# Kernel optimization log

Measured on AMD Instinct MI355X. Metric: run time of the kernel, lower is better.

## Reference

```python
import jax, jax.numpy as jnp
import numpy as np

N = 100000
E = 1600000
F_IN = 128
HID = 16
HEADS = 8
NCLS = 2
NGRAPH = 64
NEG_SLOPE = 0.2


def setup_inputs() -> dict:
    key = jax.random.key(0)
    ks = jax.random.split(key, 12)
    x = jax.random.normal(ks[0], (N, F_IN), dtype=jnp.float32)
    edge_index = jax.random.randint(ks[1], (2, E), 0, N, dtype=jnp.int64)
    batch = jnp.sort(jax.random.randint(ks[2], (N,), 0, NGRAPH, dtype=jnp.int64))
    s1 = 1.0 / np.sqrt(F_IN)
    s2 = 1.0 / np.sqrt(HEADS * HID)
    W1 = jax.random.normal(ks[3], (F_IN, HEADS * HID), dtype=jnp.float32) * s1
    att_src1 = jax.random.normal(ks[4], (HEADS, HID), dtype=jnp.float32) * s2
    att_dst1 = jax.random.normal(ks[5], (HEADS, HID), dtype=jnp.float32) * s2
    b1 = jnp.zeros((HEADS * HID,), dtype=jnp.float32)
    W2 = jax.random.normal(ks[6], (HEADS * HID, 1 * NCLS), dtype=jnp.float32) * s2
    att_src2 = jax.random.normal(ks[7], (1, NCLS), dtype=jnp.float32)
    att_dst2 = jax.random.normal(ks[8], (1, NCLS), dtype=jnp.float32)
    b2 = jnp.zeros((NCLS,), dtype=jnp.float32)
    return {"x": x, "edge_index": edge_index, "batch": batch,
            "W1": W1, "att_src1": att_src1, "att_dst1": att_dst1, "b1": b1,
            "W2": W2, "att_src2": att_src2, "att_dst2": att_dst2, "b2": b2}


def _gat_conv(x, src, dst, W, att_src, att_dst, bias, heads, out_dim, concat):
    # x: [N, Fin]; src/dst: [E'] (self-loops already appended)
    h = (x @ W).reshape(N, heads, out_dim)              # [N, H, D]
    a_src = jnp.sum(h * att_src[None], axis=-1)          # [N, H]
    a_dst = jnp.sum(h * att_dst[None], axis=-1)          # [N, H]
    e = a_src[src] + a_dst[dst]                          # [E', H]
    e = jnp.where(e >= 0, e, NEG_SLOPE * e)              # leaky_relu
    # softmax over incoming edges of each destination node
    emax = jax.ops.segment_max(e, dst, num_segments=N)   # [N, H]
    ee = jnp.exp(e - emax[dst])
    denom = jax.ops.segment_sum(ee, dst, num_segments=N)
    alpha = ee / denom[dst]                              # [E', H]
    msg = h[src] * alpha[:, :, None]                     # [E', H, D]
    out = jax.ops.segment_sum(msg, dst, num_segments=N)  # [N, H, D]
    if concat:
        out = out.reshape(N, heads * out_dim)
    else:
        out = out.mean(axis=1)
    return out + bias


def reference(x, edge_index, batch, W1, att_src1, att_dst1, b1, W2, att_src2, att_dst2, b2):
    # add self-loops (PyG GATConv default add_self_loops=True)
    loop = jnp.arange(N, dtype=edge_index.dtype)
    src = jnp.concatenate([edge_index[0], loop])
    dst = jnp.concatenate([edge_index[1], loop])

    h = _gat_conv(x, src, dst, W1, att_src1, att_dst1, b1, HEADS, HID, True)
    h = jax.nn.elu(h)
    h = _gat_conv(h, src, dst, W2, att_src2, att_dst2, b2, 1, NCLS, False)

    # global mean pool over graphs
    ssum = jax.ops.segment_sum(h, batch, num_segments=NGRAPH)          # [G, C]
    cnt = jax.ops.segment_sum(jnp.ones((N,), h.dtype), batch, num_segments=NGRAPH)
    pooled = ssum / jnp.maximum(cnt, 1.0)[:, None]
    return jax.nn.log_softmax(pooled, axis=1)
```

## Files before the change

kernel.cpp:

```cpp
#include <hip/hip_runtime.h>
#include <math.h>

typedef long long ll;
typedef unsigned int u32;
typedef unsigned short u16;

#define NBLK 256
#define MAXBUK 512

__device__ __forceinline__ int load_idx(const void* p, int i, int is64) {
  return is64 ? (int)((const ll*)p)[i] : ((const int*)p)[i];
}

__device__ __forceinline__ u16 f2bf(float f) {
  u32 u = __float_as_uint(f);
  u += 0x7FFFu + ((u >> 16) & 1u);
  return (u16)(u >> 16);
}

__global__ void detect_kernel(const void* __restrict__ eidx, int ne,
                              const void* __restrict__ batch, int nb,
                              int* __restrict__ flags) {
  if (threadIdx.x == 0 && blockIdx.x == 0) {
    int e64 = 1;
    for (int k = 1; k <= 16; ++k) {
      int i = (int)((ll)k * (ne / 2 - 1) / 16);
      ll v = ((const ll*)eidx)[i];
      if (v < 0 || v >= (1LL << 31)) { e64 = 0; break; }
    }
    int b64 = 1;
    for (int k = 1; k <= 16; ++k) {
      int i = (int)((ll)k * (nb / 2 - 1) / 16);
      ll v = ((const ll*)batch)[i];
      if (v < 0 || v >= (1LL << 31)) { b64 = 0; break; }
    }
    flags[0] = e64; flags[1] = b64;
  }
}

__global__ void zero_kernel(float* __restrict__ pool) {
  int i = threadIdx.x;
  if (i < 192) pool[i] = 0.f;
}

__global__ __launch_bounds__(256) void gemm1_kernel(
    const float* __restrict__ x, const float* __restrict__ W1,
    const float* __restrict__ att_src, const float* __restrict__ att_dst,
    u16* __restrict__ h, float* __restrict__ a_src, float* __restrict__ a_dst,
    int nn) {
  __shared__ float4 Ws[128][32];
  __shared__ float xs[32][128];
  int t = threadIdx.x;
  const float4* W4 = (const float4*)W1;
  #pragma unroll
  for (int i = 0; i < 16; ++i) {
    int f = t + i * 256;
    Ws[f >> 5][f & 31] = W4[f];
  }
  int q = t & 31, p = t >> 5;
  int n0 = blockIdx.x * 64;
  const float4 as4 = ((const float4*)att_src)[q];
  const float4 ad4 = ((const float4*)att_dst)[q];
  for (int g = 0; g < 64; g += 32) {
    __syncthreads();
    #pragma unroll
    for (int i = 0; i < 4; ++i) {
      int f = t + i * 256;
      int node = f >> 5, c4 = f & 31;
      int gn = n0 + g + node;
      float4 v = make_float4(0.f, 0.f, 0.f, 0.f);
      if (gn < nn) v = ((const float4*)x)[(size_t)gn * 32 + c4];
      *(float4*)&xs[node][c4 << 2] = v;
    }
    __syncthreads();
    float4 acc[4];
    #pragma unroll
    for (int r = 0; r < 4; ++r) acc[r] = make_float4(0.f, 0.f, 0.f, 0.f);
    #pragma unroll 4
    for (int k = 0; k < 128; ++k) {
      float4 w = Ws[k][q];
      #pragma unroll
      for (int r = 0; r < 4; ++r) {
        float xv = xs[p + r * 8][k];
        acc[r].x = fmaf(xv, w.x, acc[r].x);
        acc[r].y = fmaf(xv, w.y, acc[r].y);
        acc[r].z = fmaf(xv, w.z, acc[r].z);
        acc[r].w = fmaf(xv, w.w, acc[r].w);
      }
    }
    int head = q >> 2;
    #pragma unroll
    for (int r = 0; r < 4; ++r) {
      int n = n0 + g + p + r * 8;
      float s = acc[r].x*as4.x + acc[r].y*as4.y + acc[r].z*as4.z + acc[r].w*as4.w;
      float d = acc[r].x*ad4.x + acc[r].y*ad4.y + acc[r].z*ad4.z + acc[r].w*ad4.w;
      s += __shfl_xor(s, 1); s += __shfl_xor(s, 2);
      d += __shfl_xor(d, 1); d += __shfl_xor(d, 2);
      if (n < nn) {
        uint2 pk;
        pk.x = (u32)f2bf(acc[r].x) | ((u32)f2bf(acc[r].y) << 16);
        pk.y = (u32)f2bf(acc[r].z) | ((u32)f2bf(acc[r].w) << 16);
        ((uint2*)(h + (size_t)n * 128))[q] = pk;
        if ((q & 3) == 0) { a_src[n * 8 + head] = s; a_dst[n * 8 + head] = d; }
      }
    }
  }
}

__global__ __launch_bounds__(512) void ehist_kernel(
    const void* __restrict__ eidx, int E, int EP, int chunk,
    const int* __restrict__ flags, int* __restrict__ hist_g, int nbuk) {
  __shared__ int cnt[MAXBUK];
  int t = threadIdx.x, blk = blockIdx.x;
  if (t < MAXBUK) cnt[t] = 0;
  __syncthreads();
  int lo = blk * chunk, hi = min(lo + chunk, EP);
  int is64 = flags[0];
  for (int i = lo + t; i < hi; i += 512) {
    int d = (i < E) ? load_idx(eidx, E + i, is64) : (i - E);
    atomicAdd(&cnt[d >> 8], 1);
  }
  __syncthreads();
  if (t < nbuk) hist_g[t * NBLK + blk] = cnt[t];
}

__global__ __launch_bounds__(256) void scan_blk(const int* __restrict__ in,
                                                int* __restrict__ out,
                                                int* __restrict__ bsums, int n) {
  int t = threadIdx.x;
  int i = blockIdx.x * 256 + t;
  int v = (i < n) ? in[i] : 0;
  int lane = t & 63, w = t >> 6;
  int s = v;
  #pragma unroll
  for (int off = 1; off < 64; off <<= 1) {
    int u = __shfl_up(s, off);
    if (lane >= off) s += u;
  }
  __shared__ int wsum[4];
  if (lane == 63) wsum[w] = s;
  __syncthreads();
  int add = 0;
  for (int k = 0; k < w; ++k) add += wsum[k];
  int incl = s + add;
  if (i < n) out[i] = incl - v;
  if (t == 255) bsums[blockIdx.x] = incl;
}

__global__ __launch_bounds__(1024) void scan_top(int* __restrict__ bsums, int nb) {
  int t = threadIdx.x;
  int v = (t < nb) ? bsums[t] : 0;
  int lane = t & 63, w = t >> 6;
  int s = v;
  #pragma unroll
  for (int off = 1; off < 64; off <<= 1) {
    int u = __shfl_up(s, off);
    if (lane >= off) s += u;
  }
  __shared__ int ws[16];
  if (lane == 63) ws[w] = s;
  __syncthreads();
  int add = 0;
  for (int k = 0; k < w; ++k) add += ws[k];
  if (t < nb) bsums[t] = s + add - v;
}

__global__ void scan_add(int* __restrict__ out, const int* __restrict__ bsums, int n) {
  int i = blockIdx.x * 256 + threadIdx.x;
  if (i < n) out[i] += bsums[blockIdx.x];
}

__global__ __launch_bounds__(512) void escatter_kernel(
    const void* __restrict__ eidx, int E, int EP, int chunk,
    const int* __restrict__ flags, const int* __restrict__ base_g,
    u32* __restrict__ pairs, int nbuk) {
  __shared__ int cur[MAXBUK];
  int t = threadIdx.x, blk = blockIdx.x;
  if (t < nbuk) cur[t] = base_g[t * NBLK + blk];
  __syncthreads();
  int lo = blk * chunk, hi = min(lo + chunk, EP);
  int is64 = flags[0];
  for (int i = lo + t; i < hi; i += 512) {
    int s, d;
    if (i < E) { s = load_idx(eidx, i, is64); d = load_idx(eidx, E + i, is64); }
    else { s = d = i - E; }
    int pos = atomicAdd(&cur[d >> 8], 1);
    pairs[pos] = ((u32)(d & 255) << 24) | (u32)s;
  }
}

__global__ __launch_bounds__(256) void bfinal_kernel(
    const u32* __restrict__ pairs, const int* __restrict__ base_g,
    int* __restrict__ offs, int* __restrict__ ends, int* __restrict__ ssrc,
    int N, int EP, int nbuk) {
  int b = blockIdx.x, t = threadIdx.x;
  int nb0 = b << 8;
  __shared__ int cnt[256];
  __shared__ int cur[256];
  __shared__ int wsum[4];
  cnt[t] = 0;
  __syncthreads();
  int seg_start = base_g[b * NBLK];
  int seg_end = (b + 1 < nbuk) ? base_g[(b + 1) * NBLK] : EP;
  for (int i = seg_start + t; i < seg_end; i += 256) {
    atomicAdd(&cnt[pairs[i] >> 24], 1);
  }
  __syncthreads();
  int v = cnt[t];
  int lane = t & 63, w = t >> 6;
  int s = v;
  #pragma unroll
  for (int off = 1; off < 64; off <<= 1) {
    int u = __shfl_up(s, off);
    if (lane >= off) s += u;
  }
  if (lane == 63) wsum[w] = s;
  __syncthreads();
  int add = 0;
  for (int k = 0; k < w; ++k) add += wsum[k];
  int excl = s + add - v;
  cur[t] = excl;
  int node = nb0 + t;
  if (node < N) { offs[node] = seg_start + excl; ends[node] = seg_start + excl + v; }
  __syncthreads();
  for (int i = seg_start + t; i < seg_end; i += 256) {
    u32 p = pairs[i];
    int pos = atomicAdd(&cur[p >> 24], 1);
    ssrc[seg_start + pos] = (int)(p & 0xFFFFFFu);
  }
}

__global__ __launch_bounds__(256) void node1_kernel(
    const int* __restrict__ ssrc, const int* __restrict__ offs, const int* __restrict__ ends,
    const u16* __restrict__ h, const float* __restrict__ a_src, const float* __restrict__ a_dst,
    const float* __restrict__ b1, const float* __restrict__ W2,
    const float* __restrict__ att_s2, const float* __restrict__ att_d2,
    float* __restrict__ h2, float* __restrict__ as2, float* __restrict__ ad2, int nn) {
  int t = threadIdx.x;
  int wid = t >> 6, lane = t & 63;
  int grp = lane >> 4, lg = lane & 15;
  int n = blockIdx.x * 16 + wid * 4 + grp;
  bool nvalid = (n < nn);
  int nc = nvalid ? n : (nn - 1);
  int hh = lg >> 1;
  float adst = a_dst[nc * 8 + hh];
  int beg = offs[nc], end = ends[nc];
  int deg = nvalid ? (end - beg) : 0;
  int maxd = deg;
  maxd = max(maxd, __shfl_xor(maxd, 16));
  maxd = max(maxd, __shfl_xor(maxd, 32));
  float acc[8];
  #pragma unroll
  for (int k = 0; k < 8; ++k) acc[k] = 0.f;
  float dsum = 0.f;
  const u32* h32 = (const u32*)h;
  for (int it = 0; it < maxd; it += 4) {
    int s4[4]; float ea4[4]; uint4 v4[4];
    #pragma unroll
    for (int u = 0; u < 4; ++u) {
      int id = beg + it + u;
      s4[u] = ssrc[id < end ? id : end - 1];
    }
    #pragma unroll
    for (int u = 0; u < 4; ++u) {
      v4[u]  = *(const uint4*)(h32 + s4[u] * 64 + lg * 4);
      ea4[u] = a_src[s4[u] * 8 + hh];
    }
    #pragma unroll
    for (int u = 0; u < 4; ++u) {
      float e = ea4[u] + adst;
      e = fmaxf(e, 0.2f * e);
      float ee = (it + u < deg) ? __expf(e) : 0.f;
      dsum += ee;
      acc[0] = fmaf(ee, __uint_as_float(v4[u].x << 16),          acc[0]);
      acc[1] = fmaf(ee, __uint_as_float(v4[u].x & 0xFFFF0000u),  acc[1]);
      acc[2] = fmaf(ee, __uint_as_float(v4[u].y << 16),          acc[2]);
      acc[3] = fmaf(ee, __uint_as_float(v4[u].y & 0xFFFF0000u),  acc[3]);
      acc[4] = fmaf(ee, __uint_as_float(v4[u].z << 16),          acc[4]);
      acc[5] = fmaf(ee, __uint_as_float(v4[u].z & 0xFFFF0000u),  acc[5]);
      acc[6] = fmaf(ee, __uint_as_float(v4[u].w << 16),          acc[6]);
      acc[7] = fmaf(ee, __uint_as_float(v4[u].w & 0xFFFF0000u),  acc[7]);
    }
  }
  float inv = 1.f / dsum;
  float p0 = 0.f, p1 = 0.f;
  #pragma unroll
  for (int k = 0; k < 8; ++k) {
    int j = lg * 8 + k;
    float o = acc[k] * inv + b1[j];
    o = (o > 0.f) ? o : expm1f(o);
    p0 = fmaf(o, W2[j * 2],     p0);
    p1 = fmaf(o, W2[j * 2 + 1], p1);
  }
  #pragma unroll
  for (int m = 1; m < 16; m <<= 1) { p0 += __shfl_xor(p0, m); p1 += __shfl_xor(p1, m); }
  if (nvalid && lg == 0) {
    h2[n * 2] = p0; h2[n * 2 + 1] = p1;
    as2[n] = p0 * att_s2[0] + p1 * att_s2[1];
    ad2[n] = p0 * att_d2[0] + p1 * att_d2[1];
  }
}

__global__ __launch_bounds__(256) void node2_kernel(
    const int* __restrict__ ssrc, const int* __restrict__ offs, const int* __restrict__ ends,
    const float* __restrict__ h2, const float* __restrict__ as2, const float* __restrict__ ad2,
    const float* __restrict__ b2, const void* __restrict__ batch, const int* __restrict__ flags,
    float* __restrict__ pool, int nn) {
  __shared__ float psum[128];
  __shared__ float pcnt[64];
  int t = threadIdx.x;
  if (t < 128) psum[t] = 0.f;
  if (t < 64) pcnt[t] = 0.f;
  __syncthreads();
  int grp = t >> 3, lane8 = t & 7;
  int b64 = flags[1];
  int n = blockIdx.x * 32 + grp;
  if (n < nn) {
    float adst = ad2[n];
    int beg = offs[n], end = ends[n];
    float acc0 = 0.f, acc1 = 0.f, dsum = 0.f;
    for (int idx = beg + lane8; idx < end; idx += 8) {
      int s = ssrc[idx];
      float e = as2[s] + adst;
      e = (e < 0.f) ? 0.2f * e : e;
      float ee = __expf(e);
      float2 hv = *(const float2*)(h2 + (size_t)s * 2);
      acc0 = fmaf(ee, hv.x, acc0);
      acc1 = fmaf(ee, hv.y, acc1);
      dsum += ee;
    }
    #pragma unroll
    for (int m = 1; m < 8; m <<= 1) {
      acc0 += __shfl_xor(acc0, m);
      acc1 += __shfl_xor(acc1, m);
      dsum += __shfl_xor(dsum, m);
    }
    if (lane8 == 0) {
      float o0 = acc0 / dsum + b2[0];
      float o1 = acc1 / dsum + b2[1];
      int g = load_idx(batch, n, b64);
      atomicAdd(&psum[g * 2], o0);
      atomicAdd(&psum[g * 2 + 1], o1);
      atomicAdd(&pcnt[g], 1.f);
    }
  }
  __syncthreads();
  if (t < 64 && pcnt[t] > 0.f) {
    atomicAdd(&pool[t * 2], psum[t * 2]);
    atomicAdd(&pool[t * 2 + 1], psum[t * 2 + 1]);
    atomicAdd(&pool[128 + t], pcnt[t]);
  }
}

__global__ void finalize_kernel(const float* __restrict__ pool, float* __restrict__ out) {
  int g = threadIdx.x;
  if (g < 64) {
    float c = fmaxf(pool[128 + g], 1.f);
    float p0 = pool[g * 2] / c, p1 = pool[g * 2 + 1] / c;
    float m = fmaxf(p0, p1);
    float lse = m + logf(expf(p0 - m) + expf(p1 - m));
    out[g * 2] = p0 - lse;
    out[g * 2 + 1] = p1 - lse;
  }
}

extern "C" void kernel_launch(void* const* d_in, const int* in_sizes, int n_in,
                              void* d_out, int out_size, void* d_ws, size_t ws_size,
                              hipStream_t stream) {
  const float* x        = (const float*)d_in[0];
  const void* eidx      = d_in[1];
  const void* batch     = d_in[2];
  const float* W1       = (const float*)d_in[3];
  const float* att_src1 = (const float*)d_in[4];
  const float* att_dst1 = (const float*)d_in[5];
  const float* b1       = (const float*)d_in[6];
  const float* W2       = (const float*)d_in[7];
  const float* att_src2 = (const float*)d_in[8];
  const float* att_dst2 = (const float*)d_in[9];
  const float* b2       = (const float*)d_in[10];
  float* out = (float*)d_out;

  int N = in_sizes[0] / 128;
  int E = in_sizes[1] / 2;
  int EP = E + N;
  int NBUK = (N + 255) >> 8;
  int NC = NBUK * NBLK;
  int NB = (NC + 255) / 256;
  int chunk = (EP + NBLK - 1) / NBLK;

  char* ws = (char*)d_ws;
  size_t o = 0;
  auto alloc = [&](size_t bytes) -> void* {
    void* p = ws + o;
    o += (bytes + 255) & ~(size_t)255;
    return p;
  };
  u16*   h      = (u16*)alloc((size_t)N * 128 * 2);
  float* a_src1 = (float*)alloc((size_t)N * 8 * 4);
  float* a_dst1 = (float*)alloc((size_t)N * 8 * 4);
  int*   offs   = (int*)alloc((size_t)N * 4);
  int*   ends   = (int*)alloc((size_t)N * 4);
  int*   hist_g = (int*)alloc((size_t)NC * 4);
  int*   base_g = (int*)alloc((size_t)NC * 4);
  int*   bsums  = (int*)alloc((size_t)(NB + 1) * 4);
  u32*   pairs  = (u32*)alloc((size_t)EP * 4);
  int*   ssrc   = (int*)alloc((size_t)EP * 4);
  float* h2     = (float*)alloc((size_t)N * 2 * 4);
  float* as2    = (float*)alloc((size_t)N * 4);
  float* ad2    = (float*)alloc((size_t)N * 4);
  float* pool   = (float*)alloc(192 * 4);
  int*   flags  = (int*)alloc(2 * 4);

  detect_kernel<<<1, 64, 0, stream>>>(eidx, 2 * E, batch, N, flags);
  zero_kernel<<<1, 256, 0, stream>>>(pool);
  gemm1_kernel<<<(N + 63) / 64, 256, 0, stream>>>(x, W1, att_src1, att_dst1,
                                                  h, a_src1, a_dst1, N);
  ehist_kernel<<<NBLK, 512, 0, stream>>>(eidx, E, EP, chunk, flags, hist_g, NBUK);
  scan_blk<<<NB, 256, 0, stream>>>(hist_g, base_g, bsums, NC);
  scan_top<<<1, 1024, 0, stream>>>(bsums, NB);
  scan_add<<<NB, 256, 0, stream>>>(base_g, bsums, NC);
  escatter_kernel<<<NBLK, 512, 0, stream>>>(eidx, E, EP, chunk, flags, base_g, pairs, NBUK);
  bfinal_kernel<<<NBUK, 256, 0, stream>>>(pairs, base_g, offs, ends, ssrc, N, EP, NBUK);
  node1_kernel<<<(N + 15) / 16, 256, 0, stream>>>(ssrc, offs, ends, h, a_src1, a_dst1,
                                                  b1, W2, att_src2, att_dst2,
                                                  h2, as2, ad2, N);
  node2_kernel<<<(N + 31) / 32, 256, 0, stream>>>(ssrc, offs, ends, h2, as2, ad2,
                                                  b2, batch, flags, pool, N);
  finalize_kernel<<<1, 64, 0, stream>>>(pool, out);
}
```

Measured before the change: 244.9 us.

## Use bf16 MFMA for layer-1 GEMM and software-pipeline neighbor index loads

Replaces the scalar FP32 FMA GEMM for x@W1 with bf16 MFMA 16x16x32 instructions. x and W1 are converted to bf16 in shared memory, and results are staged through LDS to compute the attention logits and the packed bf16 h. Separately, the layer-1 aggregation loop now double-buffers source-index loads so the next group's indices are fetched while the current group is processed. This trades input precision (x and W are rounded to bf16 before the multiply) for matrix-core throughput. Each block also re-converts the whole of W1 to bf16 on entry, which adds per-block overhead.

After: 214.0 us. -12.6%, faster.

```diff
diff --git a/kernel.cpp b/kernel.cpp
--- a/kernel.cpp
+++ b/kernel.cpp
@@ -4,6 +4,8 @@
 typedef long long ll;
 typedef unsigned int u32;
 typedef unsigned short u16;
+typedef __attribute__((ext_vector_type(8))) short short8;
+typedef __attribute__((ext_vector_type(4))) float f32x4;
 
 #define NBLK 256
 #define MAXBUK 512
@@ -48,61 +50,88 @@
     const float* __restrict__ att_src, const float* __restrict__ att_dst,
     u16* __restrict__ h, float* __restrict__ a_src, float* __restrict__ a_dst,
     int nn) {
-  __shared__ float4 Ws[128][32];
-  __shared__ float xs[32][128];
+  __shared__ __align__(16) char smem[64 * 136 * 2 + 128 * 136 * 2];
+  u16* xs = (u16*)smem;
+  u16* Wt = (u16*)(smem + 64 * 136 * 2);
+  float* hs = (float*)smem;
   int t = threadIdx.x;
-  const float4* W4 = (const float4*)W1;
-  #pragma unroll
-  for (int i = 0; i < 16; ++i) {
-    int f = t + i * 256;
-    Ws[f >> 5][f & 31] = W4[f];
-  }
+  int n0 = blockIdx.x * 64;
+
+  #pragma unroll 4
+  for (int p = 0; p < 64; ++p) {
+    int i = t + p * 256;
+    int k = i >> 7, j = i & 127;
+    u16 w = f2bf(W1[i]);
+    Wt[j * 136 + k] = w;
+  }
+  #pragma unroll
+  for (int p = 0; p < 4; ++p) {
+    int row = p * 16 + (t >> 4);
+    int c = t & 15;
+    int gn = n0 + row;
+    uint4 pk = make_uint4(0u, 0u, 0u, 0u);
+    if (gn < nn) {
+      const float4* xp = (const float4*)(x + (size_t)gn * 128 + c * 8);
+      float4 f0 = xp[0], f1 = xp[1];
+      pk.x = (u32)f2bf(f0.x) | ((u32)f2bf(f0.y) << 16);
+      pk.y = (u32)f2bf(f0.z) | ((u32)f2bf(f0.w) << 16);
+      pk.z = (u32)f2bf(f1.x) | ((u32)f2bf(f1.y) << 16);
+      pk.w = (u32)f2bf(f1.z) | ((u32)f2bf(f1.w) << 16);
+    }
+    *(uint4*)&xs[row * 136 + c * 8] = pk;
+  }
+  __syncthreads();
+
+  int lane = t & 63, wid = t >> 6;
+  int lrow = lane & 15, lq = lane >> 4;
+  short8 a[4];
+  #pragma unroll
+  for (int ks = 0; ks < 4; ++ks) {
+    int row = wid * 16 + lrow;
+    a[ks] = *(const short8*)&xs[row * 136 + ks * 32 + lq * 8];
+  }
+  f32x4 c[8];
+  #pragma unroll
+  for (int jt = 0; jt < 8; ++jt) c[jt] = (f32x4)(0.f);
+  #pragma unroll
+  for (int jt = 0; jt < 8; ++jt) {
+    int j = jt * 16 + lrow;
+    #pragma unroll
+    for (int ks = 0; ks < 4; ++ks) {
+      short8 b = *(const short8*)&Wt[j * 136 + ks * 32 + lq * 8];
+      c[jt] = __builtin_amdgcn_mfma_f32_16x16x32_bf16(a[ks], b, c[jt], 0, 0, 0);
+    }
+  }
+  __syncthreads();
+
+  #pragma unroll
+  for (int jt = 0; jt < 8; ++jt) {
+    #pragma unroll
+    for (int r = 0; r < 4; ++r) {
+      hs[(wid * 16 + lq * 4 + r) * 132 + jt * 16 + lrow] = c[jt][r];
+    }
+  }
+  __syncthreads();
+
   int q = t & 31, p = t >> 5;
-  int n0 = blockIdx.x * 64;
   const float4 as4 = ((const float4*)att_src)[q];
   const float4 ad4 = ((const float4*)att_dst)[q];
-  for (int g = 0; g < 64; g += 32) {
-    __syncthreads();
-    #pragma unroll
-    for (int i = 0; i < 4; ++i) {
-      int f = t + i * 256;
-      int node = f >> 5, c4 = f & 31;
-      int gn = n0 + g + node;
-      float4 v = make_float4(0.f, 0.f, 0.f, 0.f);
-      if (gn < nn) v = ((const float4*)x)[(size_t)gn * 32 + c4];
-      *(float4*)&xs[node][c4 << 2] = v;
-    }
-    __syncthreads();
-    float4 acc[4];
-    #pragma unroll
-    for (int r = 0; r < 4; ++r) acc[r] = make_float4(0.f, 0.f, 0.f, 0.f);
-    #pragma unroll 4
-    for (int k = 0; k < 128; ++k) {
-      float4 w = Ws[k][q];
-      #pragma unroll
-      for (int r = 0; r < 4; ++r) {
-        float xv = xs[p + r * 8][k];
-        acc[r].x = fmaf(xv, w.x, acc[r].x);
-        acc[r].y = fmaf(xv, w.y, acc[r].y);
-        acc[r].z = fmaf(xv, w.z, acc[r].z);
-        acc[r].w = fmaf(xv, w.w, acc[r].w);
-      }
-    }
-    int head = q >> 2;
-    #pragma unroll
-    for (int r = 0; r < 4; ++r) {
-      int n = n0 + g + p + r * 8;
-      float s = acc[r].x*as4.x + acc[r].y*as4.y + acc[r].z*as4.z + acc[r].w*as4.w;
-      float d = acc[r].x*ad4.x + acc[r].y*ad4.y + acc[r].z*ad4.z + acc[r].w*ad4.w;
-      s += __shfl_xor(s, 1); s += __shfl_xor(s, 2);
-      d += __shfl_xor(d, 1); d += __shfl_xor(d, 2);
-      if (n < nn) {
-        uint2 pk;
-        pk.x = (u32)f2bf(acc[r].x) | ((u32)f2bf(acc[r].y) << 16);
-        pk.y = (u32)f2bf(acc[r].z) | ((u32)f2bf(acc[r].w) << 16);
-        ((uint2*)(h + (size_t)n * 128))[q] = pk;
-        if ((q & 3) == 0) { a_src[n * 8 + head] = s; a_dst[n * 8 + head] = d; }
-      }
+  int head = q >> 2;
+  #pragma unroll
+  for (int rr = 0; rr < 8; ++rr) {
+    int row = rr * 8 + p;
+    int n = n0 + row;
+    float4 v = *(const float4*)&hs[row * 132 + q * 4];
+    float s = v.x * as4.x + v.y * as4.y + v.z * as4.z + v.w * as4.w;
+    float d = v.x * ad4.x + v.y * ad4.y + v.z * ad4.z + v.w * ad4.w;
+    s += __shfl_xor(s, 1); s += __shfl_xor(s, 2);
+    d += __shfl_xor(d, 1); d += __shfl_xor(d, 2);
+    if (n < nn) {
+      uint2 pk;
+      pk.x = (u32)f2bf(v.x) | ((u32)f2bf(v.y) << 16);
+      pk.y = (u32)f2bf(v.z) | ((u32)f2bf(v.w) << 16);
+      ((uint2*)(h + (size_t)n * 128))[q] = pk;
+      if ((q & 3) == 0) { a_src[n * 8 + head] = s; a_dst[n * 8 + head] = d; }
     }
   }
 }
@@ -254,13 +283,16 @@
   for (int k = 0; k < 8; ++k) acc[k] = 0.f;
   float dsum = 0.f;
   const u32* h32 = (const u32*)h;
-  for (int it = 0; it < maxd; it += 4) {
-    int s4[4]; float ea4[4]; uint4 v4[4];
+
+  auto ld4 = [&](int* s4, int it0) {
     #pragma unroll
     for (int u = 0; u < 4; ++u) {
-      int id = beg + it + u;
+      int id = beg + it0 + u;
       s4[u] = ssrc[id < end ? id : end - 1];
     }
+  };
+  auto step = [&](const int* s4, int it0) {
+    float ea4[4]; uint4 v4[4];
     #pragma unroll
     for (int u = 0; u < 4; ++u) {
       v4[u]  = *(const uint4*)(h32 + s4[u] * 64 + lg * 4);
@@ -270,7 +302,7 @@
     for (int u = 0; u < 4; ++u) {
       float e = ea4[u] + adst;
       e = fmaxf(e, 0.2f * e);
-      float ee = (it + u < deg) ? __expf(e) : 0.f;
+      float ee = (it0 + u < deg) ? __expf(e) : 0.f;
       dsum += ee;
       acc[0] = fmaf(ee, __uint_as_float(v4[u].x << 16),          acc[0]);
       acc[1] = fmaf(ee, __uint_as_float(v4[u].x & 0xFFFF0000u),  acc[1]);
@@ -281,7 +313,19 @@
       acc[6] = fmaf(ee, __uint_as_float(v4[u].w << 16),          acc[6]);
       acc[7] = fmaf(ee, __uint_as_float(v4[u].w & 0xFFFF0000u),  acc[7]);
     }
-  }
+  };
+
+  if (maxd > 0) {
+    int sa[4], sb[4];
+    ld4(sa, 0);
+    for (int it = 0; it < maxd; it += 8) {
+      ld4(sb, it + 4);
+      step(sa, it);
+      ld4(sa, it + 8);
+      step(sb, it + 4);
+    }
+  }
+
   float inv = 1.f / dsum;
   float p0 = 0.f, p1 = 0.f;
   #pragma unroll
```
